# Kernel optimization log

Hardware: AMD Instinct MI355X
Metric: run time of the kernel (lower is better)

The kernel has to match this reference:

```python
import jax, jax.numpy as jnp
import numpy as np

B, L, E, D, H, P, NL = 4, 2048, 7, 512, 8, 720, 2
DH = D // H
FACTOR = 5
U = min(L, FACTOR * int(np.ceil(np.log(L))))  # top-u queries, = 40
SCALE = 1.0 / np.sqrt(DH)


def setup_inputs() -> dict:
    key = jax.random.key(0)
    ks = jax.random.split(key, 12)
    s = 0.02
    rn = lambda k, shape: jax.random.normal(k, shape, jnp.float32) * s
    return {
        "x": jax.random.normal(ks[0], (B, L, E), jnp.float32),
        "emb_w": rn(ks[1], (E, D)), "emb_b": jnp.zeros((D,), jnp.float32),
        "Wq": rn(ks[2], (NL, D, D)), "bq": jnp.zeros((NL, D), jnp.float32),
        "Wk": rn(ks[3], (NL, D, D)), "bk": jnp.zeros((NL, D), jnp.float32),
        "Wv": rn(ks[4], (NL, D, D)), "bv": jnp.zeros((NL, D), jnp.float32),
        "Wo": rn(ks[5], (NL, D, D)), "bo": jnp.zeros((NL, D), jnp.float32),
        "W1": rn(ks[6], (NL, D, D)), "b1": jnp.zeros((NL, D), jnp.float32),
        "W2": rn(ks[7], (NL, D, D)), "b2": jnp.zeros((NL, D), jnp.float32),
        "ln1_g": jnp.ones((NL, D), jnp.float32), "ln1_b": jnp.zeros((NL, D), jnp.float32),
        "ln2_g": jnp.ones((NL, D), jnp.float32), "ln2_b": jnp.zeros((NL, D), jnp.float32),
        "proj_w": rn(ks[8], (D, E)), "proj_b": jnp.zeros((E,), jnp.float32),
    }


def layer_norm(x, g, b):
    m = jnp.mean(x, axis=-1, keepdims=True)
    v = jnp.mean(jnp.square(x - m), axis=-1, keepdims=True)
    return (x - m) * jax.lax.rsqrt(v + 1e-5) * g + b


def prob_sparse_attn(x, Wq, bq, Wk, bk, Wv, bv, Wo, bo):
    # x: [B, L, D] -> heads [B, H, L, DH]
    q = (x @ Wq + bq).reshape(B, L, H, DH).transpose(0, 2, 1, 3)
    k = (x @ Wk + bk).reshape(B, L, H, DH).transpose(0, 2, 1, 3)
    v = (x @ Wv + bv).reshape(B, L, H, DH).transpose(0, 2, 1, 3)
    scores = jnp.einsum('bhqd,bhkd->bhqk', q, k) * SCALE  # [B,H,L,L]
    # sparsity measure M(q) = max_k - mean_k
    M = jnp.max(scores, axis=-1) - jnp.mean(scores, axis=-1)  # [B,H,L]
    _, idx = jax.lax.top_k(M, U)  # [B,H,U] indices of active queries
    s_top = jnp.take_along_axis(scores, idx[..., None], axis=2)  # [B,H,U,L]
    attn = jax.nn.softmax(s_top, axis=-1)
    upd = jnp.einsum('bhul,bhld->bhud', attn, v)  # [B,H,U,DH]
    # lazy queries get the mean of V; active queries get attention output
    ctx = jnp.broadcast_to(jnp.mean(v, axis=2, keepdims=True), v.shape)
    bidx = jnp.arange(B)[:, None, None]
    hidx = jnp.arange(H)[None, :, None]
    ctx = ctx.at[bidx, hidx, idx].set(upd)  # scatter active queries
    out = ctx.transpose(0, 2, 1, 3).reshape(B, L, D)
    return out @ Wo + bo


def reference(x, emb_w, emb_b, Wq, bq, Wk, bk, Wv, bv, Wo, bo,
              W1, b1, W2, b2, ln1_g, ln1_b, ln2_g, ln2_b, proj_w, proj_b):
    h = x @ emb_w + emb_b  # [B,L,D]
    for i in range(NL):
        a = prob_sparse_attn(h, Wq[i], bq[i], Wk[i], bk[i], Wv[i], bv[i], Wo[i], bo[i])
        h = layer_norm(h + a, ln1_g[i], ln1_b[i])
        f = jax.nn.relu(h @ W1[i] + b1[i]) @ W2[i] + b2[i]
        h = layer_norm(h + f, ln2_g[i], ln2_b[i])
    return h[:, -P:, :] @ proj_w + proj_b  # [B,P,E]
```

## Files before the change

kernel.cpp:

```cpp
#include <hip/hip_runtime.h>
#include <hip/hip_bf16.h>
#include <cstdint>
#include <cstddef>

#define BB 4
#define LL 2048
#define EE 7
#define DD 512
#define HH 8
#define DHH 64
#define PP 720
#define NLAYER 2
#define UU 40
#define SCALE 0.125f
#define ROWS (BB*LL)
#define BIGN ((size_t)ROWS*DD)
#define NIN 21
#define FCH 256
#define NCH (LL/FCH)
#define PSTR 264
#define VSTR 136

typedef unsigned short u16;
typedef unsigned long long u64;
typedef __bf16 bf16x8 __attribute__((ext_vector_type(8)));
typedef float  f32x4  __attribute__((ext_vector_type(4)));

__device__ __forceinline__ float bf2f(u16 u){
  union { uint32_t i; float f; } c; c.i = ((uint32_t)u) << 16; return c.f;
}
__device__ __forceinline__ u16 f2b(float f){
  __hip_bfloat16 h = __float2bfloat16(f);
  return *(u16*)&h;
}
__device__ __forceinline__ void gld_lds16(const u16* g, u16* l){
  __builtin_amdgcn_global_load_lds(
      (const __attribute__((address_space(1))) uint32_t*)g,
      (__attribute__((address_space(3))) uint32_t*)l, 16, 0, 0);
}
__device__ __forceinline__ int is_bf16(const void* d15){
  return (*(const uint32_t*)d15 == 0x3F800000u) ? 0 : 1;
}

#define NSMALL 15
struct ConvArgs { const void* src[NSMALL]; int off[NSMALL]; int n[NSMALL]; };
struct WPtrs { const void* p[6]; };

__global__ __launch_bounds__(256) void k_preamble(ConvArgs a, WPtrs wp,
    const void* __restrict__ xraw, const void* __restrict__ d15,
    float* __restrict__ dst, float* __restrict__ zbuf,
    u16* __restrict__ hB, u16* __restrict__ wT){
  int y = blockIdx.y, bx = blockIdx.x, t = threadIdx.x;
  int isbf = is_bf16(d15);
  __shared__ u16 tile[64][65];
  __shared__ float xs[32][EE];
  if (y < NSMALL){
    int i = bx*256 + t;
    if (i >= a.n[y]) return;
    float v;
    if (isbf) v = bf2f(((const u16*)a.src[y])[i]);
    else      v = ((const float*)a.src[y])[i];
    dst[(size_t)a.off[y] + i] = v;
  } else if (y == NSMALL){
    int i = bx*256 + t;
    if (i < NLAYER*4096) zbuf[i] = 0.f;
  } else if (y < 32){
    int flat = (y - 16)*256 + bx;
    if (flat >= 512) return;
    int colgrp = flat & 1;
    int rowbase = (flat >> 1) * 32;
    int dd = colgrp*256 + t;
    if (t < 32*EE){
      int j = t / EE, e = t - j*EE;
      xs[j][e] = isbf ? bf2f(((const u16*)xraw)[(rowbase + j)*EE + e])
                      : ((const float*)xraw)[(rowbase + j)*EE + e];
    }
    float wreg[EE];
    #pragma unroll
    for (int e=0;e<EE;e++)
      wreg[e] = isbf ? bf2f(((const u16*)a.src[1])[e*DD + dd])
                     : ((const float*)a.src[1])[e*DD + dd];
    float bias = isbf ? bf2f(((const u16*)a.src[2])[dd]) : ((const float*)a.src[2])[dd];
    __syncthreads();
    for (int j=0;j<32;j++){
      float acc = bias;
      #pragma unroll
      for (int e=0;e<EE;e++) acc = fmaf(xs[j][e], wreg[e], acc);
      hB[(size_t)(rowbase + j)*DD + dd] = f2b(acc);
    }
  } else {
    int flat = (y - 32)*256 + bx;
    int mz = flat >> 6, tl = flat & 63;
    int lay = mz / 6, mat = mz % 6;
    int n0 = (tl & 7)*64, k0 = (tl >> 3)*64;
    int r = t >> 6, c = t & 63;
    const void* src = wp.p[mat];
    for (int rr = r; rr < 64; rr += 4){
      size_t idx = ((size_t)lay*DD + (k0+rr))*DD + n0 + c;
      u16 v;
      if (isbf) v = ((const u16*)src)[idx];
      else      v = f2b(((const float*)src)[idx]);
      tile[rr][c] = v;
    }
    __syncthreads();
    u16* drow = wT + ((size_t)mz*DD + n0)*DD + k0;
    int c4 = (t & 15)*4;
    for (int rr = (t >> 4); rr < 64; rr += 16){
      ushort4 v = { tile[c4][rr], tile[c4+1][rr], tile[c4+2][rr], tile[c4+3][rr] };
      *(ushort4*)(drow + (size_t)rr*DD + c4) = v;
    }
  }
}

__global__ __launch_bounds__(256) void k_gemm_mfma(const u16* __restrict__ A, const u16* __restrict__ Bt,
    const float* __restrict__ bias, u16* __restrict__ Cb, int relu){
  __shared__ u16 As[128*64];
  __shared__ u16 Bs[128*64];
  int t = threadIdx.x, wave = t >> 6, lane = t & 63;
  int qlane = lane & 15, quad = lane >> 4;
  int flat = blockIdx.x + gridDim.x*blockIdx.y;
  int xcd = flat & 7, rest = flat >> 3;
  int mb = (xcd + 8*(rest & 7)) * 128;
  int nb = (rest >> 3) * 128;
  int wm = (wave & 1) * 64, wn = (wave >> 1) * 64;
  f32x4 acc[4][4];
  #pragma unroll
  for (int i=0;i<4;i++)
    #pragma unroll
    for (int j=0;j<4;j++) acc[i][j] = (f32x4){0.f,0.f,0.f,0.f};

  int srow = wave*8 + (lane>>3);
  int scol = (((lane&7) ^ ((lane>>3)&7))) * 8;
  const u16* Ag = A + (size_t)(mb + srow)*DD + scol;
  const u16* Bg = Bt + (size_t)(nb + srow)*DD + scol;

  for (int k0 = 0; k0 < DD; k0 += 64){
    __syncthreads();
    #pragma unroll
    for (int i=0;i<4;i++){
      gld_lds16(Ag + (size_t)i*32*DD + k0, As + (i*32 + wave*8)*64);
      gld_lds16(Bg + (size_t)i*32*DD + k0, Bs + (i*32 + wave*8)*64);
    }
    __syncthreads();
    #pragma unroll
    for (int ch=0; ch<2; ++ch){
      bf16x8 af[4], bf[4];
      int cgL = ((ch*4 + quad) ^ (qlane & 7)) * 8;
      #pragma unroll
      for (int i=0;i<4;i++) af[i] = *(const bf16x8*)(As + (wm + i*16 + qlane)*64 + cgL);
      #pragma unroll
      for (int j=0;j<4;j++) bf[j] = *(const bf16x8*)(Bs + (wn + j*16 + qlane)*64 + cgL);
      #pragma unroll
      for (int i=0;i<4;i++)
        #pragma unroll
        for (int j=0;j<4;j++)
          acc[i][j] = __builtin_amdgcn_mfma_f32_16x16x32_bf16(af[i], bf[j], acc[i][j], 0, 0, 0);
    }
  }
  #pragma unroll
  for (int i=0;i<4;i++){
    int rbase = mb + wm + i*16 + quad*4;
    #pragma unroll
    for (int j=0;j<4;j++){
      int col = nb + wn + j*16 + qlane;
      float bv = bias[col];
      #pragma unroll
      for (int r=0;r<4;r++){
        float cv = acc[i][j][r] + bv;
        if (relu) cv = fmaxf(cv, 0.f);
        Cb[(size_t)(rbase + r)*DD + col] = f2b(cv);
      }
    }
  }
}

__global__ __launch_bounds__(256) void k_gemm_wo(const u64* __restrict__ rowPtr, const u16* __restrict__ Bt,
    const float* __restrict__ bias, u16* __restrict__ Cb){
  __shared__ u16 As[128*64];
  __shared__ u16 Bs[128*64];
  int t = threadIdx.x, wave = t >> 6, lane = t & 63;
  int qlane = lane & 15, quad = lane >> 4;
  int flat = blockIdx.x + gridDim.x*blockIdx.y;
  int xcd = flat & 7, rest = flat >> 3;
  int mb = (xcd + 8*(rest & 7)) * 128;
  int nb = (rest >> 3) * 128;
  int wm = (wave & 1) * 64, wn = (wave >> 1) * 64;
  f32x4 acc[4][4];
  #pragma unroll
  for (int i=0;i<4;i++)
    #pragma unroll
    for (int j=0;j<4;j++) acc[i][j] = (f32x4){0.f,0.f,0.f,0.f};

  int srow = wave*8 + (lane>>3);
  int scol = (((lane&7) ^ ((lane>>3)&7))) * 8;
  const u16* Bg = Bt + (size_t)(nb + srow)*DD + scol;

  for (int k0 = 0; k0 < DD; k0 += 64){
    int slice = k0 >> 6;
    __syncthreads();
    #pragma unroll
    for (int i=0;i<4;i++){
      int arow = mb + i*32 + srow;
      const u16* src = (const u16*)(uintptr_t)rowPtr[(size_t)arow*8 + slice] + scol;
      gld_lds16(src, As + (i*32 + wave*8)*64);
      gld_lds16(Bg + (size_t)i*32*DD + k0, Bs + (i*32 + wave*8)*64);
    }
    __syncthreads();
    #pragma unroll
    for (int ch=0; ch<2; ++ch){
      bf16x8 af[4], bf[4];
      int cgL = ((ch*4 + quad) ^ (qlane & 7)) * 8;
      #pragma unroll
      for (int i=0;i<4;i++) af[i] = *(const bf16x8*)(As + (wm + i*16 + qlane)*64 + cgL);
      #pragma unroll
      for (int j=0;j<4;j++) bf[j] = *(const bf16x8*)(Bs + (wn + j*16 + qlane)*64 + cgL);
      #pragma unroll
      for (int i=0;i<4;i++)
        #pragma unroll
        for (int j=0;j<4;j++)
          acc[i][j] = __builtin_amdgcn_mfma_f32_16x16x32_bf16(af[i], bf[j], acc[i][j], 0, 0, 0);
    }
  }
  #pragma unroll
  for (int i=0;i<4;i++){
    int rbase = mb + wm + i*16 + quad*4;
    #pragma unroll
    for (int j=0;j<4;j++){
      int col = nb + wn + j*16 + qlane;
      float bv = bias[col];
      #pragma unroll
      for (int r=0;r<4;r++){
        float cv = acc[i][j][r] + bv;
        Cb[(size_t)(rbase + r)*DD + col] = f2b(cv);
      }
    }
  }
}

__global__ __launch_bounds__(256) void k_gemm_qkv(const u16* __restrict__ A, const u16* __restrict__ Wt,
    const float* __restrict__ bq, const float* __restrict__ bk, const float* __restrict__ bv,
    u16* __restrict__ qB, u16* __restrict__ kB, u16* __restrict__ vB,
    float* __restrict__ ksum, float* __restrict__ vsum){
  __shared__ u16 As[128*64];
  __shared__ u16 Bs[128*64];
  int t = threadIdx.x, wave = t >> 6, lane = t & 63;
  int qlane = lane & 15, quad = lane >> 4;
  int flat = blockIdx.x + gridDim.x*blockIdx.y;
  int xcd = flat & 7, rest = flat >> 3;
  int mb  = (xcd + 8*(rest & 7)) * 128;
  int nbg = (rest >> 3) * 128;
  int sel = nbg >> 9;
  int nb  = nbg & 511;
  const float* bias = (sel==0) ? bq : (sel==1) ? bk : bv;
  u16* out = (sel==0) ? qB : (sel==1) ? kB : vB;
  const u16* Bt = Wt + (size_t)sel*DD*DD;
  int wm = (wave & 1) * 64, wn = (wave >> 1) * 64;
  f32x4 acc[4][4];
  #pragma unroll
  for (int i=0;i<4;i++)
    #pragma unroll
    for (int j=0;j<4;j++) acc[i][j] = (f32x4){0.f,0.f,0.f,0.f};

  int srow = wave*8 + (lane>>3);
  int scol = (((lane&7) ^ ((lane>>3)&7))) * 8;
  const u16* Ag = A + (size_t)(mb + srow)*DD + scol;
  const u16* Bg = Bt + (size_t)(nb + srow)*DD + scol;

  for (int k0 = 0; k0 < DD; k0 += 64){
    __syncthreads();
    #pragma unroll
    for (int i=0;i<4;i++){
      gld_lds16(Ag + (size_t)i*32*DD + k0, As + (i*32 + wave*8)*64);
      gld_lds16(Bg + (size_t)i*32*DD + k0, Bs + (i*32 + wave*8)*64);
    }
    __syncthreads();
    #pragma unroll
    for (int ch=0; ch<2; ++ch){
      bf16x8 af[4], bf[4];
      int cgL = ((ch*4 + quad) ^ (qlane & 7)) * 8;
      #pragma unroll
      for (int i=0;i<4;i++) af[i] = *(const bf16x8*)(As + (wm + i*16 + qlane)*64 + cgL);
      #pragma unroll
      for (int j=0;j<4;j++) bf[j] = *(const bf16x8*)(Bs + (wn + j*16 + qlane)*64 + cgL);
      #pragma unroll
      for (int i=0;i<4;i++)
        #pragma unroll
        for (int j=0;j<4;j++)
          acc[i][j] = __builtin_amdgcn_mfma_f32_16x16x32_bf16(af[i], bf[j], acc[i][j], 0, 0, 0);
    }
  }
  float csum[4] = {0.f,0.f,0.f,0.f};
  #pragma unroll
  for (int j=0;j<4;j++){
    int col = nb + wn + j*16 + qlane;
    float bvv = bias[col];
    #pragma unroll
    for (int i=0;i<4;i++){
      int rbase = mb + wm + i*16 + quad*4;
      #pragma unroll
      for (int r=0;r<4;r++){
        float cv = acc[i][j][r] + bvv;
        out[(size_t)(rbase + r)*DD + col] = f2b(cv);
        csum[j] += cv;
      }
    }
  }
  if (sel > 0){
    float* dst = (sel==1) ? ksum : vsum;
    int bidx = mb >> 11;
    #pragma unroll
    for (int j=0;j<4;j++){
      float v = csum[j];
      v += __shfl_xor(v, 16);
      v += __shfl_xor(v, 32);
      if ((lane>>4) == 0)
        atomicAdd(dst + bidx*512 + nb + wn + j*16 + lane, v);
    }
  }
}

__global__ __launch_bounds__(256) void k_sparsity_mfma(const u16* __restrict__ qB, const u16* __restrict__ kB,
    const float* __restrict__ ksum, float* __restrict__ Mout){
  int bh = blockIdx.y; int b = bh >> 3, hh = bh & 7;
  int q0 = blockIdx.x * 64;
  int t = threadIdx.x, wave = t >> 6, lane = t & 63;
  const u16* qbase = qB + ((size_t)(b*LL + q0))*DD + hh*DHH;
  const u16* kbase = kB + ((size_t)b*LL)*DD + hh*DHH;
  bf16x8 qa[4][2];
  #pragma unroll
  for (int i=0;i<4;i++)
    #pragma unroll
    for (int c=0;c<2;c++)
      qa[i][c] = *(const bf16x8*)(qbase + (size_t)(i*16 + (lane&15))*DD + c*32 + (lane>>4)*8);
  float rmax[4][4];
  #pragma unroll
  for (int i=0;i<4;i++)
    #pragma unroll
    for (int r=0;r<4;r++) rmax[i][r] = -3.0e38f;
  for (int kt = wave*16; kt < LL; kt += 64){
    bf16x8 kb0 = *(const bf16x8*)(kbase + (size_t)(kt + (lane&15))*DD + (lane>>4)*8);
    bf16x8 kb1 = *(const bf16x8*)(kbase + (size_t)(kt + (lane&15))*DD + 32 + (lane>>4)*8);
    #pragma unroll
    for (int i=0;i<4;i++){
      f32x4 a = (f32x4){0.f,0.f,0.f,0.f};
      a = __builtin_amdgcn_mfma_f32_16x16x32_bf16(qa[i][0], kb0, a, 0, 0, 0);
      a = __builtin_amdgcn_mfma_f32_16x16x32_bf16(qa[i][1], kb1, a, 0, 0, 0);
      #pragma unroll
      for (int r=0;r<4;r++) rmax[i][r] = fmaxf(rmax[i][r], a[r]);
    }
  }
  #pragma unroll
  for (int i=0;i<4;i++)
    #pragma unroll
    for (int r=0;r<4;r++){
      float v = rmax[i][r];
      v = fmaxf(v, __shfl_xor(v, 1));
      v = fmaxf(v, __shfl_xor(v, 2));
      v = fmaxf(v, __shfl_xor(v, 4));
      v = fmaxf(v, __shfl_xor(v, 8));
      rmax[i][r] = v;
    }
  __shared__ float smax[4][64];
  if ((lane & 15) == 0){
    #pragma unroll
    for (int i=0;i<4;i++)
      #pragma unroll
      for (int r=0;r<4;r++)
        smax[wave][i*16 + (lane>>4)*4 + r] = rmax[i][r];
  }
  __syncthreads();
  if (t < 64){
    float mx = fmaxf(fmaxf(smax[0][t], smax[1][t]), fmaxf(smax[2][t], smax[3][t]));
    const u16* qrow = qB + (size_t)(b*LL + q0 + t)*DD + hh*DHH;
    float dot = 0.f;
    #pragma unroll 16
    for (int d=0; d<DHH; ++d) dot += bf2f(qrow[d]) * ksum[bh*DHH + d];
    Mout[bh*LL + q0 + t] = SCALE * (mx - dot * (1.0f/LL));
  }
}

__global__ __launch_bounds__(256) void k_flash(const u16* __restrict__ qB, const u16* __restrict__ kB,
    const u16* __restrict__ vB, const float* __restrict__ Mv, int* __restrict__ sidx,
    float* __restrict__ pO, float* __restrict__ pM, float* __restrict__ pS){
  int bh = blockIdx.y, c = blockIdx.x;
  int b = bh >> 3, hh = bh & 7;
  int t = threadIdx.x, w = t >> 6, lane = t & 63;
  int qlane = lane & 15, quad = lane >> 4;
  int l0 = c * FCH;
  __shared__ u16 Ps[48*PSTR];
  __shared__ union { uint32_t keys[LL]; u16 vst[64*VSTR]; } uu;
  __shared__ float wred[4][48];
  __shared__ float mrow[48];
  __shared__ int hist[256];
  __shared__ int scr[2];
  __shared__ int tieIdx[64];
  __shared__ int counters[2];
  __shared__ int sidxL[UU], sidxS[UU];

  {
    const float* src = Mv + (size_t)bh*LL;
    #pragma unroll
    for (int j = 0; j < 8; ++j){
      int idx = t + j*256;
      uint32_t u = __float_as_uint(src[idx]);
      uu.keys[idx] = (u & 0x80000000u) ? ~u : (u | 0x80000000u);
    }
    uint32_t prefix = 0, pmask = 0;
    int need = UU;
    #pragma unroll
    for (int pass = 0; pass < 4; ++pass){
      int shift = 24 - pass*8;
      __syncthreads();
      hist[t] = 0;
      __syncthreads();
      #pragma unroll
      for (int j = 0; j < 8; ++j){
        uint32_t k = uu.keys[t + j*256];
        if ((k & pmask) == prefix)
          atomicAdd(&hist[(k >> shift) & 0xFF], 1);
      }
      __syncthreads();
      if (t < 64){
        int ln = t;
        int h0 = hist[ln*4+0], h1 = hist[ln*4+1], h2 = hist[ln*4+2], h3 = hist[ln*4+3];
        int s = h0 + h1 + h2 + h3;
        int acc = s;
        #pragma unroll
        for (int off = 1; off < 64; off <<= 1){
          int v = __shfl_down(acc, off);
          if (ln + off < 64) acc += v;
        }
        int c3 = acc - s;
        int c2 = c3 + h3;
        int c1 = c2 + h2;
        int c0 = c1 + h1;
        if      (need > c3 && need <= c3 + h3){ scr[0] = ln*4+3; scr[1] = c3; }
        else if (need > c2 && need <= c2 + h2){ scr[0] = ln*4+2; scr[1] = c2; }
        else if (need > c1 && need <= c1 + h1){ scr[0] = ln*4+1; scr[1] = c1; }
        else if (need > c0 && need <= c0 + h0){ scr[0] = ln*4+0; scr[1] = c0; }
      }
      __syncthreads();
      prefix |= ((uint32_t)scr[0]) << shift;
      need -= scr[1];
      pmask |= 0xFFu << shift;
    }
    if (t < 2) counters[t] = 0;
    __syncthreads();
    uint32_t Tkey = prefix;
    #pragma unroll
    for (int j = 0; j < 8; ++j){
      int idx = t + j*256;
      uint32_t k = uu.keys[idx];
      if (k > Tkey){
        int p = atomicAdd(&counters[0], 1);
        sidxL[p] = idx;
      } else if (k == Tkey){
        int p = atomicAdd(&counters[1], 1);
        if (p < 64) tieIdx[p] = idx;
      }
    }
    __syncthreads();
    if (t == 0){
      int c_gt = counters[0];
      int tc = counters[1];
      int needTies = UU - c_gt;
      if (tc <= 64){
        for (int m = 0; m < needTies; ++m){
          int bestv = 0x7FFFFFFF, bestp = -1;
          for (int q = 0; q < tc; ++q)
            if (tieIdx[q] < bestv){ bestv = tieIdx[q]; bestp = q; }
          sidxL[c_gt + m] = bestv;
          tieIdx[bestp] = 0x7FFFFFFF;
        }
      } else {
        int m = 0;
        for (int j = 0; j < LL && m < needTies; ++j)
          if (uu.keys[j] == Tkey){ sidxL[c_gt + m] = j; m++; }
      }
    }
    __syncthreads();
    int vv = 0, rk = 0;
    if (t < UU){
      vv = sidxL[t];
      #pragma unroll 8
      for (int j = 0; j < UU; ++j) rk += (sidxL[j] < vv) ? 1 : 0;
    }
    __syncthreads();
    if (t < UU) sidxS[rk] = vv;
    __syncthreads();
    if (c == 0 && t < UU) sidx[bh*UU + t] = sidxS[t];
  }

  const u16* kbase = kB + (size_t)b*LL*DD + hh*DHH;
  const u16* vbase = vB + (size_t)b*LL*DD + hh*DHH;
  const u16* qbase = qB + (size_t)b*LL*DD + hh*DHH;

  bf16x8 qa[3][2];
  #pragma unroll
  for (int i=0;i<3;i++){
    int u = i*16 + qlane;
    if (u < UU){
      const u16* qr = qbase + (size_t)sidxS[u]*DD + quad*8;
      qa[i][0] = *(const bf16x8*)qr;
      qa[i][1] = *(const bf16x8*)(qr + 32);
    } else {
      bf16x8 z;
      #pragma unroll
      for (int q8=0;q8<8;q8++) z[q8] = (__bf16)0.0f;
      qa[i][0] = z; qa[i][1] = z;
    }
  }
  f32x4 S[3][4];
  #pragma unroll
  for (int j=0;j<4;j++){
    const u16* kr = kbase + (size_t)(l0 + w*64 + j*16 + qlane)*DD + quad*8;
    bf16x8 k0 = *(const bf16x8*)kr;
    bf16x8 k1 = *(const bf16x8*)(kr + 32);
    #pragma unroll
    for (int i=0;i<3;i++){
      f32x4 a = (f32x4){0.f,0.f,0.f,0.f};
      a = __builtin_amdgcn_mfma_f32_16x16x32_bf16(qa[i][0], k0, a, 0, 0, 0);
      a = __builtin_amdgcn_mfma_f32_16x16x32_bf16(qa[i][1], k1, a, 0, 0, 0);
      S[i][j] = a;
    }
  }
  #pragma unroll
  for (int i=0;i<3;i++){
    #pragma unroll
    for (int r=0;r<4;r++){
      float m = -3.0e38f;
      #pragma unroll
      for (int j=0;j<4;j++){ S[i][j][r] *= SCALE; m = fmaxf(m, S[i][j][r]); }
      m = fmaxf(m, __shfl_xor(m, 1));
      m = fmaxf(m, __shfl_xor(m, 2));
      m = fmaxf(m, __shfl_xor(m, 4));
      m = fmaxf(m, __shfl_xor(m, 8));
      if (qlane == 0) wred[w][i*16 + quad*4 + r] = m;
    }
  }
  __syncthreads();
  if (t < 48) mrow[t] = fmaxf(fmaxf(wred[0][t], wred[1][t]), fmaxf(wred[2][t], wred[3][t]));
  __syncthreads();
  #pragma unroll
  for (int i=0;i<3;i++){
    #pragma unroll
    for (int r=0;r<4;r++){
      int row = i*16 + quad*4 + r;
      float m = mrow[row];
      float ls = 0.f;
      #pragma unroll
      for (int j=0;j<4;j++){
        float e = __expf(S[i][j][r] - m);
        ls += e;
        Ps[row*PSTR + w*64 + j*16 + qlane] = f2b(e);
      }
      ls += __shfl_xor(ls, 1);
      ls += __shfl_xor(ls, 2);
      ls += __shfl_xor(ls, 4);
      ls += __shfl_xor(ls, 8);
      if (qlane == 0) wred[w][row] = ls;
    }
  }
  __syncthreads();
  if (t < 48){
    pM[(bh*NCH + c)*48 + t] = mrow[t];
    pS[(bh*NCH + c)*48 + t] = wred[0][t] + wred[1][t] + wred[2][t] + wred[3][t];
  }
  f32x4 O[3];
  #pragma unroll
  for (int i=0;i<3;i++) O[i] = (f32x4){0.f,0.f,0.f,0.f};
  for (int half = 0; half < 2; ++half){
    __syncthreads();
    for (int idx = t; idx < 128*64; idx += 256){
      int rr = idx >> 6, d = idx & 63;
      uu.vst[d*VSTR + rr] = vbase[(size_t)(l0 + half*128 + rr)*DD + d];
    }
    __syncthreads();
    #pragma unroll
    for (int ks = 0; ks < 4; ++ks){
      int kloc = half*128 + ks*32;
      bf16x8 bfv = *(const bf16x8*)(uu.vst + (w*16 + qlane)*VSTR + ks*32 + quad*8);
      #pragma unroll
      for (int i=0;i<3;i++){
        bf16x8 af = *(const bf16x8*)(Ps + (i*16 + qlane)*PSTR + kloc + quad*8);
        O[i] = __builtin_amdgcn_mfma_f32_16x16x32_bf16(af, bfv, O[i], 0, 0, 0);
      }
    }
  }
  size_t ob = (size_t)(bh*NCH + c)*48*64;
  #pragma unroll
  for (int i=0;i<3;i++)
    #pragma unroll
    for (int r=0;r<4;r++)
      pO[ob + (size_t)(i*16 + quad*4 + r)*64 + w*16 + qlane] = O[i][r];
}

__global__ __launch_bounds__(256) void k_flash_red(const float* __restrict__ pO, const float* __restrict__ pM,
    const float* __restrict__ pS, const int* __restrict__ sidx, const float* __restrict__ vsum,
    u16* __restrict__ attnC, u16* __restrict__ vmeanB, u64* __restrict__ rowPtr){
  int bh = blockIdx.x; int b = bh >> 3, hh = bh & 7;
  int t = threadIdx.x;
  if (t < 64) vmeanB[b*512 + hh*64 + t] = f2b(vsum[b*512 + hh*64 + t] * (1.0f/LL));
  u64 vmPtr = (u64)(uintptr_t)(vmeanB + b*512 + hh*64);
  for (int row = t; row < LL; row += 256)
    rowPtr[((size_t)b*LL + row)*8 + hh] = vmPtr;
  __syncthreads();
  if (t < UU)
    rowPtr[((size_t)b*LL + sidx[bh*UU + t])*8 + hh] =
        (u64)(uintptr_t)(attnC + ((size_t)bh*UU + t)*64);
  for (int idx = t; idx < UU*64; idx += 256){
    int u = idx >> 6, n = idx & 63;
    float m = -3.0e38f;
    #pragma unroll
    for (int c=0;c<NCH;c++) m = fmaxf(m, pM[(bh*NCH + c)*48 + u]);
    float s = 0.f, o = 0.f;
    #pragma unroll
    for (int c=0;c<NCH;c++){
      float wgt = __expf(pM[(bh*NCH + c)*48 + u] - m);
      s += wgt * pS[(bh*NCH + c)*48 + u];
      o += wgt * pO[((size_t)(bh*NCH + c)*48 + u)*64 + n];
    }
    attnC[((size_t)bh*UU + u)*64 + n] = f2b(o / s);
  }
}

__global__ __launch_bounds__(256) void k_addln(const u16* __restrict__ a, const u16* __restrict__ r,
    const float* __restrict__ g, const float* __restrict__ bvec, u16* __restrict__ outB){
  int row = blockIdx.x*4 + (threadIdx.x >> 6);
  int lane = threadIdx.x & 63;
  size_t base = (size_t)row * DD + lane*8;
  ushort4 a0 = *(const ushort4*)(a + base);
  ushort4 a1 = *(const ushort4*)(a + base + 4);
  ushort4 r0 = *(const ushort4*)(r + base);
  ushort4 r1 = *(const ushort4*)(r + base + 4);
  float x[8] = {bf2f(a0.x)+bf2f(r0.x), bf2f(a0.y)+bf2f(r0.y),
                bf2f(a0.z)+bf2f(r0.z), bf2f(a0.w)+bf2f(r0.w),
                bf2f(a1.x)+bf2f(r1.x), bf2f(a1.y)+bf2f(r1.y),
                bf2f(a1.z)+bf2f(r1.z), bf2f(a1.w)+bf2f(r1.w)};
  float s = 0.f;
  #pragma unroll
  for (int i=0;i<8;i++) s += x[i];
  #pragma unroll
  for (int off=1; off<64; off<<=1) s += __shfl_xor(s, off);
  float mean = s * (1.0f/DD);
  float vs = 0.f;
  #pragma unroll
  for (int i=0;i<8;i++){ x[i] -= mean; vs += x[i]*x[i]; }
  #pragma unroll
  for (int off=1; off<64; off<<=1) vs += __shfl_xor(vs, off);
  float rs = rsqrtf(vs * (1.0f/DD) + 1e-5f);
  const float* gp = g + lane*8;
  const float* bp = bvec + lane*8;
  u16 ob[8];
  #pragma unroll
  for (int i=0;i<8;i++) ob[i] = f2b(x[i]*rs*gp[i] + bp[i]);
  *(ushort4*)(outB + base)     = (ushort4){ob[0],ob[1],ob[2],ob[3]};
  *(ushort4*)(outB + base + 4) = (ushort4){ob[4],ob[5],ob[6],ob[7]};
}

__global__ __launch_bounds__(64) void k_proj(const u16* __restrict__ hB, const float* __restrict__ pw,
    const float* __restrict__ pb, void* __restrict__ out, const void* __restrict__ d15){
  int rp = blockIdx.x; int b = rp / PP, pp = rp % PP;
  int t = threadIdx.x;
  const u16* hr = hB + (size_t)(b*LL + (LL-PP) + pp) * DD;
  float acc[EE];
  #pragma unroll
  for (int e=0;e<EE;e++) acc[e]=0.f;
  for (int d = t; d < DD; d += 64){
    float hv = bf2f(hr[d]);
    #pragma unroll
    for (int e=0;e<EE;e++) acc[e] = fmaf(hv, pw[d*EE+e], acc[e]);
  }
  int isbf = is_bf16(d15);
  #pragma unroll
  for (int e=0;e<EE;e++){
    float rr = acc[e];
    for (int off=32; off>0; off>>=1) rr += __shfl_down(rr, off);
    if (t == 0){
      float val = rr + pb[e];
      if (isbf) ((__hip_bfloat16*)out)[(size_t)rp*EE + e] = __float2bfloat16(val);
      else      ((float*)out)[(size_t)rp*EE + e] = val;
    }
  }
}

extern "C" void kernel_launch(void* const* d_in, const int* in_sizes, int n_in,
                              void* d_out, int out_size, void* d_ws, size_t ws_size,
                              hipStream_t stream){
  float* ws    = (float*)d_ws;
  float* Mv    = ws;
  float* ksumL = Mv + (size_t)BB*HH*LL;
  float* pM    = ksumL + NLAYER*4096;
  float* pS    = pM + 12288;
  float* pO    = pS + 12288;
  int*   sidx  = (int*)(pO + 786432);
  u64*   rowPtr= (u64*)(((uintptr_t)(sidx + 1280) + 15) & ~(uintptr_t)15);
  u16*   attnC = (u16*)(rowPtr + (size_t)ROWS*8);
  u16*   vmeanB= attnC + (size_t)BB*HH*UU*64;
  u16*   hB    = vmeanB + 2048;
  u16*   qB    = hB + BIGN;
  u16*   kB    = qB + BIGN;
  u16*   vB    = kB + BIGN;
  u16*   f1B   = vB + BIGN;
  u16*   tmpB  = f1B + BIGN;
  u16*   wT    = tmpB + BIGN;
  float* conv  = (float*)(((uintptr_t)(wT + (size_t)12*DD*DD) + 15) & ~(uintptr_t)15);

  static const int small_ids[NSMALL] = {0,1,2,4,6,8,10,12,14,15,16,17,18,19,20};
  ConvArgs ca;
  int off_all[NIN];
  int tot = 0;
  for (int i = 0; i < NIN; ++i) off_all[i] = -1;
  for (int s = 0; s < NSMALL; ++s){
    int i = small_ids[s];
    ca.src[s] = d_in[i];
    ca.off[s] = tot;
    ca.n[s]   = in_sizes[i];
    off_all[i] = tot;
    tot += in_sizes[i];
  }
  const float* bq = conv + off_all[4];
  const float* bk = conv + off_all[6];
  const float* bv = conv + off_all[8];
  const float* bo = conv + off_all[10];
  const float* b1 = conv + off_all[12];
  const float* b2 = conv + off_all[14];
  const float* ln1g = conv + off_all[15]; const float* ln1b = conv + off_all[16];
  const float* ln2g = conv + off_all[17]; const float* ln2b = conv + off_all[18];
  const float* pw = conv + off_all[19]; const float* pb = conv + off_all[20];

  WPtrs wp;
  wp.p[0]=d_in[3]; wp.p[1]=d_in[5]; wp.p[2]=d_in[7];
  wp.p[3]=d_in[9]; wp.p[4]=d_in[11]; wp.p[5]=d_in[13];

  k_preamble<<<dim3(256, 35), 256, 0, stream>>>(ca, wp, d_in[0], d_in[15],
                                                conv, ksumL, hB, wT);

  dim3 gg(DD/128, ROWS/128);
  dim3 gq(3*DD/128, ROWS/128);

  for (int l = 0; l < NLAYER; ++l){
    const u16* WqkvT = wT + (size_t)(l*6 + 0)*DD*DD;
    const u16* WoT   = wT + (size_t)(l*6 + 3)*DD*DD;
    const u16* W1T   = wT + (size_t)(l*6 + 4)*DD*DD;
    const u16* W2T   = wT + (size_t)(l*6 + 5)*DD*DD;
    float* ksum = ksumL + l*4096;
    float* vsum = ksum + 2048;

    k_gemm_qkv<<<gq, 256, 0, stream>>>(hB, WqkvT, bq + l*DD, bk + l*DD, bv + l*DD,
                                       qB, kB, vB, ksum, vsum);
    k_sparsity_mfma<<<dim3(LL/64, BB*HH), 256, 0, stream>>>(qB, kB, ksum, Mv);
    k_flash<<<dim3(NCH, BB*HH), 256, 0, stream>>>(qB, kB, vB, Mv, sidx, pO, pM, pS);
    k_flash_red<<<BB*HH, 256, 0, stream>>>(pO, pM, pS, sidx, vsum, attnC, vmeanB, rowPtr);
    k_gemm_wo<<<gg, 256, 0, stream>>>(rowPtr, WoT, bo + l*DD, tmpB);
    k_addln<<<ROWS/4, 256, 0, stream>>>(hB, tmpB, ln1g + l*DD, ln1b + l*DD, hB);
    k_gemm_mfma<<<gg, 256, 0, stream>>>(hB, W1T, b1 + l*DD, f1B, 1);
    k_gemm_mfma<<<gg, 256, 0, stream>>>(f1B, W2T, b2 + l*DD, tmpB, 0);
    k_addln<<<ROWS/4, 256, 0, stream>>>(hB, tmpB, ln2g + l*DD, ln2b + l*DD, hB);
  }
  k_proj<<<BB*PP, 64, 0, stream>>>(hB, pw, pb, d_out, d_in[15]);
}
```

Baseline: 393.0 us.

## Shrink GEMM M-tile to 64, widen sparsity query tile, repack proj kernel

The Wo/W1/W2 GEMMs move from 128x128 to 64x128 tiles, doubling the block count (512 instead of 256) so more CUs stay busy, at the cost of lower per-block reuse. The sparsity kernel now handles 128 queries per block with an XCD-aware block mapping, which reuses each K tile loaded from memory across more MFMAs, and it vectorizes the q·ksum dot product. The projection kernel packs four rows per 256-thread block and does vector loads, cutting launch and block overhead. Register pressure in the sparsity kernel rises with the larger query tile.

```diff
diff --git a/kernel.cpp b/kernel.cpp
--- a/kernel.cpp
+++ b/kernel.cpp
@@ -114,18 +114,18 @@
 
 __global__ __launch_bounds__(256) void k_gemm_mfma(const u16* __restrict__ A, const u16* __restrict__ Bt,
     const float* __restrict__ bias, u16* __restrict__ Cb, int relu){
-  __shared__ u16 As[128*64];
+  __shared__ u16 As[64*64];
   __shared__ u16 Bs[128*64];
   int t = threadIdx.x, wave = t >> 6, lane = t & 63;
   int qlane = lane & 15, quad = lane >> 4;
   int flat = blockIdx.x + gridDim.x*blockIdx.y;
   int xcd = flat & 7, rest = flat >> 3;
-  int mb = (xcd + 8*(rest & 7)) * 128;
-  int nb = (rest >> 3) * 128;
-  int wm = (wave & 1) * 64, wn = (wave >> 1) * 64;
-  f32x4 acc[4][4];
-  #pragma unroll
-  for (int i=0;i<4;i++)
+  int mb = (xcd + 8*(rest & 15)) * 64;
+  int nb = (rest >> 4) * 128;
+  int wm = (wave & 1) * 32, wn = (wave >> 1) * 64;
+  f32x4 acc[2][4];
+  #pragma unroll
+  for (int i=0;i<2;i++)
     #pragma unroll
     for (int j=0;j<4;j++) acc[i][j] = (f32x4){0.f,0.f,0.f,0.f};
 
@@ -137,28 +137,29 @@
   for (int k0 = 0; k0 < DD; k0 += 64){
     __syncthreads();
     #pragma unroll
-    for (int i=0;i<4;i++){
+    for (int i=0;i<2;i++)
       gld_lds16(Ag + (size_t)i*32*DD + k0, As + (i*32 + wave*8)*64);
+    #pragma unroll
+    for (int i=0;i<4;i++)
       gld_lds16(Bg + (size_t)i*32*DD + k0, Bs + (i*32 + wave*8)*64);
-    }
     __syncthreads();
     #pragma unroll
     for (int ch=0; ch<2; ++ch){
-      bf16x8 af[4], bf[4];
+      bf16x8 af[2], bfv[4];
       int cgL = ((ch*4 + quad) ^ (qlane & 7)) * 8;
       #pragma unroll
-      for (int i=0;i<4;i++) af[i] = *(const bf16x8*)(As + (wm + i*16 + qlane)*64 + cgL);
-      #pragma unroll
-      for (int j=0;j<4;j++) bf[j] = *(const bf16x8*)(Bs + (wn + j*16 + qlane)*64 + cgL);
-      #pragma unroll
-      for (int i=0;i<4;i++)
+      for (int i=0;i<2;i++) af[i] = *(const bf16x8*)(As + (wm + i*16 + qlane)*64 + cgL);
+      #pragma unroll
+      for (int j=0;j<4;j++) bfv[j] = *(const bf16x8*)(Bs + (wn + j*16 + qlane)*64 + cgL);
+      #pragma unroll
+      for (int i=0;i<2;i++)
         #pragma unroll
         for (int j=0;j<4;j++)
-          acc[i][j] = __builtin_amdgcn_mfma_f32_16x16x32_bf16(af[i], bf[j], acc[i][j], 0, 0, 0);
-    }
-  }
-  #pragma unroll
-  for (int i=0;i<4;i++){
+          acc[i][j] = __builtin_amdgcn_mfma_f32_16x16x32_bf16(af[i], bfv[j], acc[i][j], 0, 0, 0);
+    }
+  }
+  #pragma unroll
+  for (int i=0;i<2;i++){
     int rbase = mb + wm + i*16 + quad*4;
     #pragma unroll
     for (int j=0;j<4;j++){
@@ -176,18 +177,18 @@
 
 __global__ __launch_bounds__(256) void k_gemm_wo(const u64* __restrict__ rowPtr, const u16* __restrict__ Bt,
     const float* __restrict__ bias, u16* __restrict__ Cb){
-  __shared__ u16 As[128*64];
+  __shared__ u16 As[64*64];
   __shared__ u16 Bs[128*64];
   int t = threadIdx.x, wave = t >> 6, lane = t & 63;
   int qlane = lane & 15, quad = lane >> 4;
   int flat = blockIdx.x + gridDim.x*blockIdx.y;
   int xcd = flat & 7, rest = flat >> 3;
-  int mb = (xcd + 8*(rest & 7)) * 128;
-  int nb = (rest >> 3) * 128;
-  int wm = (wave & 1) * 64, wn = (wave >> 1) * 64;
-  f32x4 acc[4][4];
-  #pragma unroll
-  for (int i=0;i<4;i++)
+  int mb = (xcd + 8*(rest & 15)) * 64;
+  int nb = (rest >> 4) * 128;
+  int wm = (wave & 1) * 32, wn = (wave >> 1) * 64;
+  f32x4 acc[2][4];
+  #pragma unroll
+  for (int i=0;i<2;i++)
     #pragma unroll
     for (int j=0;j<4;j++) acc[i][j] = (f32x4){0.f,0.f,0.f,0.f};
 
@@ -199,30 +200,32 @@
     int slice = k0 >> 6;
     __syncthreads();
     #pragma unroll
-    for (int i=0;i<4;i++){
+    for (int i=0;i<2;i++){
       int arow = mb + i*32 + srow;
       const u16* src = (const u16*)(uintptr_t)rowPtr[(size_t)arow*8 + slice] + scol;
       gld_lds16(src, As + (i*32 + wave*8)*64);
+    }
+    #pragma unroll
+    for (int i=0;i<4;i++)
       gld_lds16(Bg + (size_t)i*32*DD + k0, Bs + (i*32 + wave*8)*64);
-    }
     __syncthreads();
     #pragma unroll
     for (int ch=0; ch<2; ++ch){
-      bf16x8 af[4], bf[4];
+      bf16x8 af[2], bfv[4];
       int cgL = ((ch*4 + quad) ^ (qlane & 7)) * 8;
       #pragma unroll
-      for (int i=0;i<4;i++) af[i] = *(const bf16x8*)(As + (wm + i*16 + qlane)*64 + cgL);
-      #pragma unroll
-      for (int j=0;j<4;j++) bf[j] = *(const bf16x8*)(Bs + (wn + j*16 + qlane)*64 + cgL);
-      #pragma unroll
-      for (int i=0;i<4;i++)
+      for (int i=0;i<2;i++) af[i] = *(const bf16x8*)(As + (wm + i*16 + qlane)*64 + cgL);
+      #pragma unroll
+      for (int j=0;j<4;j++) bfv[j] = *(const bf16x8*)(Bs + (wn + j*16 + qlane)*64 + cgL);
+      #pragma unroll
+      for (int i=0;i<2;i++)
         #pragma unroll
         for (int j=0;j<4;j++)
-          acc[i][j] = __builtin_amdgcn_mfma_f32_16x16x32_bf16(af[i], bf[j], acc[i][j], 0, 0, 0);
-    }
-  }
-  #pragma unroll
-  for (int i=0;i<4;i++){
+          acc[i][j] = __builtin_amdgcn_mfma_f32_16x16x32_bf16(af[i], bfv[j], acc[i][j], 0, 0, 0);
+    }
+  }
+  #pragma unroll
+  for (int i=0;i<2;i++){
     int rbase = mb + wm + i*16 + quad*4;
     #pragma unroll
     for (int j=0;j<4;j++){
@@ -321,27 +324,31 @@
 
 __global__ __launch_bounds__(256) void k_sparsity_mfma(const u16* __restrict__ qB, const u16* __restrict__ kB,
     const float* __restrict__ ksum, float* __restrict__ Mout){
-  int bh = blockIdx.y; int b = bh >> 3, hh = bh & 7;
-  int q0 = blockIdx.x * 64;
+  int flat = blockIdx.x + gridDim.x*blockIdx.y;
+  int xcd = flat & 7, rest = flat >> 3;
+  int qc = rest & 15;
+  int bh = (rest >> 4)*8 + xcd;
+  int b = bh >> 3, hh = bh & 7;
+  int q0 = qc * 128;
   int t = threadIdx.x, wave = t >> 6, lane = t & 63;
   const u16* qbase = qB + ((size_t)(b*LL + q0))*DD + hh*DHH;
   const u16* kbase = kB + ((size_t)b*LL)*DD + hh*DHH;
-  bf16x8 qa[4][2];
-  #pragma unroll
-  for (int i=0;i<4;i++)
+  bf16x8 qa[8][2];
+  #pragma unroll
+  for (int i=0;i<8;i++)
     #pragma unroll
     for (int c=0;c<2;c++)
       qa[i][c] = *(const bf16x8*)(qbase + (size_t)(i*16 + (lane&15))*DD + c*32 + (lane>>4)*8);
-  float rmax[4][4];
-  #pragma unroll
-  for (int i=0;i<4;i++)
+  float rmax[8][4];
+  #pragma unroll
+  for (int i=0;i<8;i++)
     #pragma unroll
     for (int r=0;r<4;r++) rmax[i][r] = -3.0e38f;
   for (int kt = wave*16; kt < LL; kt += 64){
     bf16x8 kb0 = *(const bf16x8*)(kbase + (size_t)(kt + (lane&15))*DD + (lane>>4)*8);
     bf16x8 kb1 = *(const bf16x8*)(kbase + (size_t)(kt + (lane&15))*DD + 32 + (lane>>4)*8);
     #pragma unroll
-    for (int i=0;i<4;i++){
+    for (int i=0;i<8;i++){
       f32x4 a = (f32x4){0.f,0.f,0.f,0.f};
       a = __builtin_amdgcn_mfma_f32_16x16x32_bf16(qa[i][0], kb0, a, 0, 0, 0);
       a = __builtin_amdgcn_mfma_f32_16x16x32_bf16(qa[i][1], kb1, a, 0, 0, 0);
@@ -350,7 +357,7 @@
     }
   }
   #pragma unroll
-  for (int i=0;i<4;i++)
+  for (int i=0;i<8;i++)
     #pragma unroll
     for (int r=0;r<4;r++){
       float v = rmax[i][r];
@@ -360,21 +367,26 @@
       v = fmaxf(v, __shfl_xor(v, 8));
       rmax[i][r] = v;
     }
-  __shared__ float smax[4][64];
+  __shared__ float smax[4][128];
   if ((lane & 15) == 0){
     #pragma unroll
-    for (int i=0;i<4;i++)
+    for (int i=0;i<8;i++)
       #pragma unroll
       for (int r=0;r<4;r++)
         smax[wave][i*16 + (lane>>4)*4 + r] = rmax[i][r];
   }
   __syncthreads();
-  if (t < 64){
+  if (t < 128){
     float mx = fmaxf(fmaxf(smax[0][t], smax[1][t]), fmaxf(smax[2][t], smax[3][t]));
     const u16* qrow = qB + (size_t)(b*LL + q0 + t)*DD + hh*DHH;
     float dot = 0.f;
-    #pragma unroll 16
-    for (int d=0; d<DHH; ++d) dot += bf2f(qrow[d]) * ksum[bh*DHH + d];
+    #pragma unroll
+    for (int dv=0; dv<16; ++dv){
+      ushort4 qv = *(const ushort4*)(qrow + dv*4);
+      const float* kp = ksum + bh*DHH + dv*4;
+      dot += bf2f(qv.x)*kp[0] + bf2f(qv.y)*kp[1]
+           + bf2f(qv.z)*kp[2] + bf2f(qv.w)*kp[3];
+    }
     Mout[bh*LL + q0 + t] = SCALE * (mx - dot * (1.0f/LL));
   }
 }
@@ -658,25 +670,32 @@
   *(ushort4*)(outB + base + 4) = (ushort4){ob[4],ob[5],ob[6],ob[7]};
 }
 
-__global__ __launch_bounds__(64) void k_proj(const u16* __restrict__ hB, const float* __restrict__ pw,
+__global__ __launch_bounds__(256) void k_proj(const u16* __restrict__ hB, const float* __restrict__ pw,
     const float* __restrict__ pb, void* __restrict__ out, const void* __restrict__ d15){
-  int rp = blockIdx.x; int b = rp / PP, pp = rp % PP;
-  int t = threadIdx.x;
-  const u16* hr = hB + (size_t)(b*LL + (LL-PP) + pp) * DD;
+  int rp = blockIdx.x*4 + (threadIdx.x >> 6);
+  int lane = threadIdx.x & 63;
+  int b = rp / PP, pp = rp - b*PP;
+  const u16* hr = hB + (size_t)(b*LL + (LL-PP) + pp) * DD + lane*8;
+  ushort4 v0 = *(const ushort4*)hr;
+  ushort4 v1 = *(const ushort4*)(hr + 4);
+  float x[8] = {bf2f(v0.x), bf2f(v0.y), bf2f(v0.z), bf2f(v0.w),
+                bf2f(v1.x), bf2f(v1.y), bf2f(v1.z), bf2f(v1.w)};
   float acc[EE];
   #pragma unroll
   for (int e=0;e<EE;e++) acc[e]=0.f;
-  for (int d = t; d < DD; d += 64){
-    float hv = bf2f(hr[d]);
-    #pragma unroll
-    for (int e=0;e<EE;e++) acc[e] = fmaf(hv, pw[d*EE+e], acc[e]);
+  #pragma unroll
+  for (int j=0;j<8;j++){
+    const float* wrow = pw + (size_t)(lane*8 + j)*EE;
+    #pragma unroll
+    for (int e=0;e<EE;e++) acc[e] = fmaf(x[j], wrow[e], acc[e]);
   }
   int isbf = is_bf16(d15);
   #pragma unroll
   for (int e=0;e<EE;e++){
     float rr = acc[e];
+    #pragma unroll
     for (int off=32; off>0; off>>=1) rr += __shfl_down(rr, off);
-    if (t == 0){
+    if (lane == 0){
       float val = rr + pb[e];
       if (isbf) ((__hip_bfloat16*)out)[(size_t)rp*EE + e] = __float2bfloat16(val);
       else      ((float*)out)[(size_t)rp*EE + e] = val;
@@ -736,7 +755,7 @@
   k_preamble<<<dim3(256, 35), 256, 0, stream>>>(ca, wp, d_in[0], d_in[15],
                                                 conv, ksumL, hB, wT);
 
-  dim3 gg(DD/128, ROWS/128);
+  dim3 gg(4, 128);
   dim3 gq(3*DD/128, ROWS/128);
 
   for (int l = 0; l < NLAYER; ++l){
@@ -749,7 +768,7 @@
 
     k_gemm_qkv<<<gq, 256, 0, stream>>>(hB, WqkvT, bq + l*DD, bk + l*DD, bv + l*DD,
                                        qB, kB, vB, ksum, vsum);
-    k_sparsity_mfma<<<dim3(LL/64, BB*HH), 256, 0, stream>>>(qB, kB, ksum, Mv);
+    k_sparsity_mfma<<<dim3(LL/128, BB*HH), 256, 0, stream>>>(qB, kB, ksum, Mv);
     k_flash<<<dim3(NCH, BB*HH), 256, 0, stream>>>(qB, kB, vB, Mv, sidx, pO, pM, pS);
     k_flash_red<<<BB*HH, 256, 0, stream>>>(pO, pM, pS, sidx, vsum, attnC, vmeanB, rowPtr);
     k_gemm_wo<<<gg, 256, 0, stream>>>(rowPtr, WoT, bo + l*DD, tmpB);
@@ -758,5 +777,5 @@
     k_gemm_mfma<<<gg, 256, 0, stream>>>(f1B, W2T, b2 + l*DD, tmpB, 0);
     k_addln<<<ROWS/4, 256, 0, stream>>>(hB, tmpB, ln2g + l*DD, ln2b + l*DD, hB);
   }
-  k_proj<<<BB*PP, 64, 0, stream>>>(hB, pw, pb, d_out, d_in[15]);
-}
+  k_proj<<<(BB*PP)/4, 256, 0, stream>>>(hB, pw, pb, d_out, d_in[15]);
+}
```

Result: faster. 362.3 us (-7.8%).
